# Performance work log

Hardware: AMD Instinct MI355X
Metric: run time of the kernel (lower is better)

The kernel has to match this reference:

```python
import jax, jax.numpy as jnp
import numpy as np

B, C, CI, HM, HC = 4, 64, 32, 128, 64  # batch, in_channels, inter_channels, main HW, cross HW
BN_EPS = 1e-5


def conv1x1(x, w, b):
    # x: [B,Cin,H,W], w: [Cout,Cin], b: [Cout]
    return jnp.einsum('bchw,oc->bohw', x, w) + b[None, :, None, None]


def _lin_coords(n_in, n_out):
    # PyTorch bilinear, align_corners=False: src = (i+0.5)*scale - 0.5, clamped
    scale = n_in / n_out
    src = (jnp.arange(n_out, dtype=jnp.float32) + 0.5) * scale - 0.5
    src = jnp.clip(src, 0.0, n_in - 1)
    i0 = jnp.floor(src).astype(jnp.int32)
    i1 = jnp.minimum(i0 + 1, n_in - 1)
    w = src - i0.astype(jnp.float32)
    return i0, i1, w


def resize_bilinear(x, h_out, w_out):
    # x: [B,C,H,W] -> [B,C,h_out,w_out], matches torch F.interpolate(mode='bilinear', align_corners=False)
    _, _, h_in, w_in = x.shape
    i0, i1, wh = _lin_coords(h_in, h_out)
    x = x[:, :, i0, :] * (1.0 - wh)[None, None, :, None] + x[:, :, i1, :] * wh[None, None, :, None]
    j0, j1, ww = _lin_coords(w_in, w_out)
    x = x[:, :, :, j0] * (1.0 - ww)[None, None, None, :] + x[:, :, :, j1] * ww[None, None, None, :]
    return x


def setup_inputs() -> dict:
    key = jax.random.key(0)
    ks = jax.random.split(key, 12)
    p = lambda k, shape, s=0.05: jax.random.normal(k, shape, dtype=jnp.float32) * s
    return {
        'main_feature': jax.random.normal(ks[0], (B, C, HM, HM), dtype=jnp.float32),
        'cross_feature': jax.random.normal(ks[1], (B, C, HC, HC), dtype=jnp.float32),
        'g_w': p(ks[2], (CI, C)), 'g_b': p(ks[3], (CI,)),
        'theta_w': p(ks[4], (CI, C)), 'theta_b': p(ks[5], (CI,)),
        'phi_w': p(ks[6], (CI, C)), 'phi_b': p(ks[7], (CI,)),
        'w_w': p(ks[8], (C, CI)), 'w_b': p(ks[9], (C,)),
        'bn_gamma': 1.0 + p(ks[10], (C,)), 'bn_beta': p(ks[11], (C,)),
    }


def reference(main_feature, cross_feature, g_w, g_b, theta_w, theta_b,
              phi_w, phi_b, w_w, w_b, bn_gamma, bn_beta):
    b, _, hc, wc = cross_feature.shape
    hm = main_feature.shape[2]
    # g(cross) -> [B, Nc, Ci]
    x = conv1x1(cross_feature, g_w, g_b).reshape(b, CI, -1).transpose(0, 2, 1)
    # theta(cross) -> [B, Ci, Nc]
    y = conv1x1(cross_feature, theta_w, theta_b).reshape(b, CI, -1)
    # phi(resize(main -> cross size)) -> [B, Nc, Ci]
    z = resize_bilinear(main_feature, hc, hc)
    z = conv1x1(z, phi_w, phi_b).reshape(b, CI, -1).transpose(0, 2, 1)
    # unscaled attention: [B, Nc, Nc]
    f = jnp.einsum('bnc,bcm->bnm', x, y)
    attn = jax.nn.softmax(f, axis=-1)
    out = jnp.einsum('bnm,bmc->bnc', attn, z)           # [B, Nc, Ci]
    out = out.transpose(0, 2, 1).reshape(b, CI, hc, wc)  # [B, Ci, Hc, Wc]
    # W: 1x1 conv + BatchNorm2d (training mode: batch statistics, biased var)
    out = conv1x1(out, w_w, w_b)
    mean = out.mean(axis=(0, 2, 3), keepdims=True)
    var = out.var(axis=(0, 2, 3), keepdims=True)
    out = (out - mean) * jax.lax.rsqrt(var + BN_EPS)
    out = out * bn_gamma[None, :, None, None] + bn_beta[None, :, None, None]
    out = resize_bilinear(out, hm, hm)
    return out + main_feature
```

## Files before the change

kernel.cpp:

```cpp
#include <hip/hip_runtime.h>
#include <hip/hip_bf16.h>


typedef __attribute__((ext_vector_type(8))) short bf16x8;
typedef __attribute__((ext_vector_type(4))) float f32x4;
typedef __attribute__((ext_vector_type(16))) float f32x16;

#define LOG2E 1.4426950408889634f

static __device__ __forceinline__ unsigned short f2bf_bits(float x) {
    __hip_bfloat16 h = __float2bfloat16(x);
    return *(unsigned short*)&h;
}
static __device__ __forceinline__ unsigned int pk2bf(float a, float b) {
    __hip_bfloat162 h = __float22bfloat162_rn(make_float2(a, b));
    return *(unsigned int*)&h;
}

static __device__ __forceinline__ void softmax_pack(
    const f32x16& s, float& den, bf16x8& ap1, bf16x8& ap2)
{
    float e[16];
#pragma unroll
    for (int r = 0; r < 16; ++r) e[r] = __builtin_amdgcn_exp2f(s[r]);
    den += (((e[0]+e[1])+(e[2]+e[3])) + ((e[4]+e[5])+(e[6]+e[7])))
         + (((e[8]+e[9])+(e[10]+e[11])) + ((e[12]+e[13])+(e[14]+e[15])));
    uint4 t1 = make_uint4(pk2bf(e[0],e[1]), pk2bf(e[2],e[3]),
                          pk2bf(e[4],e[5]), pk2bf(e[6],e[7]));
    uint4 t2 = make_uint4(pk2bf(e[8],e[9]), pk2bf(e[10],e[11]),
                          pk2bf(e[12],e[13]), pk2bf(e[14],e[15]));
    ap1 = *(bf16x8*)&t1; ap2 = *(bf16x8*)&t2;
}

__global__ __launch_bounds__(256) void qkv_kernel(
    const float* __restrict__ cross, const float* __restrict__ mainf,
    const float* __restrict__ g_w,  const float* __restrict__ g_b,
    const float* __restrict__ th_w, const float* __restrict__ th_b,
    const float* __restrict__ ph_w, const float* __restrict__ ph_b,
    __hip_bfloat16* __restrict__ Qb, __hip_bfloat16* __restrict__ Kf,
    __hip_bfloat16* __restrict__ Vf)
{
    __shared__ __align__(16) float xs[64][128];
    const int kind = blockIdx.x >> 7;
    const int sub  = blockIdx.x & 127;
    const int b    = sub >> 5;
    const int n0   = (sub & 31) << 7;
    const int tid  = threadIdx.x;
    const float* w  = (kind == 0) ? g_w : (kind == 1) ? th_w : ph_w;
    const float* bs = (kind == 0) ? g_b : (kind == 1) ? th_b : ph_b;

    if (kind < 2) {
        const float* src = cross + (((size_t)(b * 64)) << 12) + n0;
        const int jr = (tid & 31) << 2, c0 = tid >> 5;
#pragma unroll
        for (int it = 0; it < 8; ++it) {
            int c = (it << 3) | c0;
            *(float4*)&xs[c][jr] = *(const float4*)(src + ((size_t)c << 12) + jr);
        }
    } else {
        const int px = tid & 127, chh = tid >> 7;
        const int n = n0 + px;
        const int i2 = (n >> 6) << 1, j2 = (n & 63) << 1;
        const float* src = mainf + (((size_t)(b * 64)) << 14) + i2 * 128 + j2;
#pragma unroll 4
        for (int cc = 0; cc < 32; ++cc) {
            int c = (chh << 5) | cc;
            const float2 a = *(const float2*)(src + ((size_t)c << 14));
            const float2 d = *(const float2*)(src + ((size_t)c << 14) + 128);
            xs[c][px] = 0.25f * ((a.x + a.y) + (d.x + d.y));
        }
    }
    __syncthreads();

    if (kind < 2) {
        const int px = tid & 127, cih = tid >> 7, ci0 = cih << 4;
        float acc[16];
#pragma unroll
        for (int j = 0; j < 16; ++j) acc[j] = bs[ci0 + j];
#pragma unroll 4
        for (int c = 0; c < 64; ++c) {
            float x = xs[c][px];
#pragma unroll
            for (int j = 0; j < 16; ++j)
                acc[j] = fmaf(w[((ci0 + j) << 6) + c], x, acc[j]);
        }
        const int n = n0 + px;
        const int chunk = n >> 5, kk = n & 31;
        if (kind == 0) {
#pragma unroll
            for (int j = 0; j < 16; ++j) acc[j] *= LOG2E;
            unsigned int u[8];
#pragma unroll
            for (int i = 0; i < 8; ++i)
                u[i] = (unsigned int)f2bf_bits(acc[2 * i]) |
                       ((unsigned int)f2bf_bits(acc[2 * i + 1]) << 16);
            uint4* d4 = (uint4*)(Qb + (size_t)((b << 12) + n) * 32 + ci0);
            d4[0] = make_uint4(u[0], u[1], u[2], u[3]);
            d4[1] = make_uint4(u[4], u[5], u[6], u[7]);
        } else {
            unsigned int u[8];
#pragma unroll
            for (int i = 0; i < 8; ++i)
                u[i] = (unsigned int)f2bf_bits(acc[2 * i]) |
                       ((unsigned int)f2bf_bits(acc[2 * i + 1]) << 16);
            const int q = (kk & ~12) | ((kk & 4) << 1) | ((kk & 8) >> 1);
            char* base = (char*)Kf + ((((size_t)(b << 7) | chunk) << 11) | (cih << 10));
            *(uint4*)(base + (q << 4))          = make_uint4(u[0], u[1], u[2], u[3]);
            *(uint4*)(base + ((32 + q) << 4))   = make_uint4(u[4], u[5], u[6], u[7]);
        }
    } else {
        const int cip = tid & 15, o = tid >> 4;
        const int c0 = cip << 1;
        const int pxb = o << 3;
        float a0[8], a1[8];
        const float b0 = bs[c0], b1 = bs[c0 + 1];
#pragma unroll
        for (int i = 0; i < 8; ++i) { a0[i] = b0; a1[i] = b1; }
#pragma unroll 4
        for (int c = 0; c < 64; ++c) {
            const float w0 = w[(c0 << 6) + c], w1 = w[((c0 + 1) << 6) + c];
            const float4 xa = *(const float4*)&xs[c][pxb];
            const float4 xb = *(const float4*)&xs[c][pxb + 4];
            a0[0] = fmaf(w0, xa.x, a0[0]); a0[1] = fmaf(w0, xa.y, a0[1]);
            a0[2] = fmaf(w0, xa.z, a0[2]); a0[3] = fmaf(w0, xa.w, a0[3]);
            a0[4] = fmaf(w0, xb.x, a0[4]); a0[5] = fmaf(w0, xb.y, a0[5]);
            a0[6] = fmaf(w0, xb.z, a0[6]); a0[7] = fmaf(w0, xb.w, a0[7]);
            a1[0] = fmaf(w1, xa.x, a1[0]); a1[1] = fmaf(w1, xa.y, a1[1]);
            a1[2] = fmaf(w1, xa.z, a1[2]); a1[3] = fmaf(w1, xa.w, a1[3]);
            a1[4] = fmaf(w1, xb.x, a1[4]); a1[5] = fmaf(w1, xb.y, a1[5]);
            a1[6] = fmaf(w1, xb.z, a1[6]); a1[7] = fmaf(w1, xb.w, a1[7]);
        }
        unsigned int u0[4], u1[4];
#pragma unroll
        for (int i = 0; i < 4; ++i) {
            u0[i] = (unsigned int)f2bf_bits(a0[2 * i]) |
                    ((unsigned int)f2bf_bits(a0[2 * i + 1]) << 16);
            u1[i] = (unsigned int)f2bf_bits(a1[2 * i]) |
                    ((unsigned int)f2bf_bits(a1[2 * i + 1]) << 16);
        }
        const int n = n0 + pxb;
        const int chunk = n >> 5;
        const int j = (o >> 1) & 1, hh = o & 1;
        char* base = (char*)Vf + (((size_t)((b << 7) | chunk)) << 11)
                   + (j << 10) + (hh << 9) + (c0 << 4);
        *(uint4*)base        = make_uint4(u0[0], u0[1], u0[2], u0[3]);
        *(uint4*)(base + 16) = make_uint4(u1[0], u1[1], u1[2], u1[3]);
    }
}

__global__ __launch_bounds__(256) void attn_part(
    const __hip_bfloat16* __restrict__ Qb, const __hip_bfloat16* __restrict__ Kf,
    const __hip_bfloat16* __restrict__ Vf,
    float* __restrict__ pnum, float* __restrict__ pden)
{
    __shared__ __align__(16) float redbuf[4][3][64][16];
    __shared__ float denarr[4][3][64];
    const int tid = threadIdx.x, lane = tid & 63, w = tid >> 6;
    const int q = lane & 31, h = lane >> 5;
    const int b = blockIdx.y, qbase = blockIdx.x << 7, eighth = blockIdx.z;

    const __hip_bfloat16* QrowA = Qb + (((size_t)(b << 12) + qbase + q) << 5);
    const bf16x8 bq1A = *(const bf16x8*)(QrowA + 8 * h);
    const bf16x8 bq2A = *(const bf16x8*)(QrowA + 16 + 8 * h);
    const bf16x8 bq1B = *(const bf16x8*)(QrowA + (32 << 5) + 8 * h);
    const bf16x8 bq2B = *(const bf16x8*)(QrowA + (32 << 5) + 16 + 8 * h);
    const bf16x8 bq1C = *(const bf16x8*)(QrowA + (64 << 5) + 8 * h);
    const bf16x8 bq2C = *(const bf16x8*)(QrowA + (64 << 5) + 16 + 8 * h);
    const bf16x8 bq1D = *(const bf16x8*)(QrowA + (96 << 5) + 8 * h);
    const bf16x8 bq2D = *(const bf16x8*)(QrowA + (96 << 5) + 16 + 8 * h);

    const char* Kc = (const char*)Kf +
        ((size_t)((b << 7) | (eighth << 4) | (w << 2)) << 11) + (lane << 4);
    const char* Vc = (const char*)Vf +
        ((size_t)((b << 7) | (eighth << 4) | (w << 2)) << 11) + (lane << 4);
#define LDK1(c) (*(const bf16x8*)(Kc + ((c) << 11)))
#define LDK2(c) (*(const bf16x8*)(Kc + ((c) << 11) + 1024))
#define LDV1(c) (*(const bf16x8*)(Vc + ((c) << 11)))
#define LDV2(c) (*(const bf16x8*)(Vc + ((c) << 11) + 1024))

    f32x16 accA, accB, accC, accD;
#pragma unroll
    for (int r = 0; r < 16; ++r) { accA[r]=0.f; accB[r]=0.f; accC[r]=0.f; accD[r]=0.f; }
    const f32x16 z16 = accA;
    float denA = 0.f, denB = 0.f, denC = 0.f, denD = 0.f;

    bf16x8 a1c = LDK1(0), a2c = LDK2(0);
    bf16x8 vb1 = LDV1(0), vb2 = LDV2(0);
    bf16x8 a1n = LDK1(1), a2n = LDK2(1);
    bf16x8 vn1 = LDV1(1), vn2 = LDV2(1);
    bf16x8 apA1, apA2, apB1, apB2, apC1, apC2, apD1, apD2, vp1, vp2;

    {
        f32x16 s = __builtin_amdgcn_mfma_f32_32x32x16_bf16(a1c, bq1A, z16, 0, 0, 0);
        s = __builtin_amdgcn_mfma_f32_32x32x16_bf16(a2c, bq2A, s, 0, 0, 0);
        softmax_pack(s, denA, apA1, apA2);
        s = __builtin_amdgcn_mfma_f32_32x32x16_bf16(a1c, bq1B, z16, 0, 0, 0);
        s = __builtin_amdgcn_mfma_f32_32x32x16_bf16(a2c, bq2B, s, 0, 0, 0);
        softmax_pack(s, denB, apB1, apB2);
        s = __builtin_amdgcn_mfma_f32_32x32x16_bf16(a1c, bq1C, z16, 0, 0, 0);
        s = __builtin_amdgcn_mfma_f32_32x32x16_bf16(a2c, bq2C, s, 0, 0, 0);
        softmax_pack(s, denC, apC1, apC2);
        s = __builtin_amdgcn_mfma_f32_32x32x16_bf16(a1c, bq1D, z16, 0, 0, 0);
        s = __builtin_amdgcn_mfma_f32_32x32x16_bf16(a2c, bq2D, s, 0, 0, 0);
        softmax_pack(s, denD, apD1, apD2);
    }

#pragma unroll
    for (int ch = 1; ch < 4; ++ch) {
        const int kn = (ch + 1) & 3;
        vp1 = vb1; vp2 = vb2;
        vb1 = vn1; vb2 = vn2;
        a1c = a1n; a2c = a2n;
        a1n = LDK1(kn); a2n = LDK2(kn);
        vn1 = LDV1(kn); vn2 = LDV2(kn);

        accA = __builtin_amdgcn_mfma_f32_32x32x16_bf16(apA1, vp1, accA, 0, 0, 0);
        accA = __builtin_amdgcn_mfma_f32_32x32x16_bf16(apA2, vp2, accA, 0, 0, 0);
        accB = __builtin_amdgcn_mfma_f32_32x32x16_bf16(apB1, vp1, accB, 0, 0, 0);
        accB = __builtin_amdgcn_mfma_f32_32x32x16_bf16(apB2, vp2, accB, 0, 0, 0);
        accC = __builtin_amdgcn_mfma_f32_32x32x16_bf16(apC1, vp1, accC, 0, 0, 0);
        accC = __builtin_amdgcn_mfma_f32_32x32x16_bf16(apC2, vp2, accC, 0, 0, 0);
        accD = __builtin_amdgcn_mfma_f32_32x32x16_bf16(apD1, vp1, accD, 0, 0, 0);
        accD = __builtin_amdgcn_mfma_f32_32x32x16_bf16(apD2, vp2, accD, 0, 0, 0);

        f32x16 s = __builtin_amdgcn_mfma_f32_32x32x16_bf16(a1c, bq1A, z16, 0, 0, 0);
        s = __builtin_amdgcn_mfma_f32_32x32x16_bf16(a2c, bq2A, s, 0, 0, 0);
        softmax_pack(s, denA, apA1, apA2);
        s = __builtin_amdgcn_mfma_f32_32x32x16_bf16(a1c, bq1B, z16, 0, 0, 0);
        s = __builtin_amdgcn_mfma_f32_32x32x16_bf16(a2c, bq2B, s, 0, 0, 0);
        softmax_pack(s, denB, apB1, apB2);
        s = __builtin_amdgcn_mfma_f32_32x32x16_bf16(a1c, bq1C, z16, 0, 0, 0);
        s = __builtin_amdgcn_mfma_f32_32x32x16_bf16(a2c, bq2C, s, 0, 0, 0);
        softmax_pack(s, denC, apC1, apC2);
        s = __builtin_amdgcn_mfma_f32_32x32x16_bf16(a1c, bq1D, z16, 0, 0, 0);
        s = __builtin_amdgcn_mfma_f32_32x32x16_bf16(a2c, bq2D, s, 0, 0, 0);
        softmax_pack(s, denD, apD1, apD2);
    }
    accA = __builtin_amdgcn_mfma_f32_32x32x16_bf16(apA1, vb1, accA, 0, 0, 0);
    accA = __builtin_amdgcn_mfma_f32_32x32x16_bf16(apA2, vb2, accA, 0, 0, 0);
    accB = __builtin_amdgcn_mfma_f32_32x32x16_bf16(apB1, vb1, accB, 0, 0, 0);
    accB = __builtin_amdgcn_mfma_f32_32x32x16_bf16(apB2, vb2, accB, 0, 0, 0);
    accC = __builtin_amdgcn_mfma_f32_32x32x16_bf16(apC1, vb1, accC, 0, 0, 0);
    accC = __builtin_amdgcn_mfma_f32_32x32x16_bf16(apC2, vb2, accC, 0, 0, 0);
    accD = __builtin_amdgcn_mfma_f32_32x32x16_bf16(apD1, vb1, accD, 0, 0, 0);
    accD = __builtin_amdgcn_mfma_f32_32x32x16_bf16(apD2, vb2, accD, 0, 0, 0);
#undef LDK1
#undef LDK2
#undef LDV1
#undef LDV2

    denA += __shfl_xor(denA, 32);
    denB += __shfl_xor(denB, 32);
    denC += __shfl_xor(denC, 32);
    denD += __shfl_xor(denD, 32);

    if (w) {
        float d[4] = {denA, denB, denC, denD};
        const f32x16* av[4] = {&accA, &accB, &accC, &accD};
#pragma unroll
        for (int T = 0; T < 4; ++T) {
            float* rb = &redbuf[T][w - 1][lane][0];
            f32x4* rb4 = (f32x4*)rb;
            const f32x16& a = *av[T];
#pragma unroll
            for (int p = 0; p < 4; ++p) {
                f32x4 t = {a[4*p], a[4*p+1], a[4*p+2], a[4*p+3]};
                rb4[p] = t;
            }
            denarr[T][w - 1][lane] = d[T];
        }
    }
    __syncthreads();
    if (w == 0) {
        const int tbase = (((eighth << 2) | b) << 7) | (blockIdx.x << 2);
        float d[4] = {denA, denB, denC, denD};
        f32x16* av[4] = {&accA, &accB, &accC, &accD};
#pragma unroll
        for (int T = 0; T < 4; ++T) {
            f32x16& a = *av[T];
#pragma unroll
            for (int ww = 0; ww < 3; ++ww) {
                const float* rb = &redbuf[T][ww][lane][0];
                const f32x4* rb4 = (const f32x4*)rb;
#pragma unroll
                for (int p = 0; p < 4; ++p) {
                    f32x4 t = rb4[p];
                    a[4*p] += t[0]; a[4*p+1] += t[1];
                    a[4*p+2] += t[2]; a[4*p+3] += t[3];
                }
                d[T] += denarr[T][ww][lane];
            }
            float* pn = pnum + ((size_t)(tbase + T) << 10);
#pragma unroll
            for (int r = 0; r < 16; ++r) {
                int qr = (r & 3) + 8 * (r >> 2) + 4 * h;
                pn[(qr << 5) + q] = a[r];
            }
            if (h == 0) pden[((tbase + T) << 5) + q] = d[T];
        }
    }
}

__global__ __launch_bounds__(256) void attn_combine(
    const float* __restrict__ pnum, const float* __restrict__ pden,
    const float* __restrict__ w_w, const float* __restrict__ w_b,
    float* __restrict__ out2, float2* __restrict__ pstats)
{
    __shared__ __align__(16) float obuf[32][36];
    const int tid = threadIdx.x;
    const int b = blockIdx.y, qbase = blockIdx.x << 5;

#pragma unroll
    for (int k = 0; k < 4; ++k) {
        int e = tid + (k << 8);
        int qr = e >> 5;
        float num = 0.f, den = 0.f;
#pragma unroll
        for (int eighth = 0; eighth < 8; ++eighth) {
            int tile = (((eighth << 2) | b) << 7) | blockIdx.x;
            num += pnum[((size_t)tile << 10) + e];
            den += pden[(tile << 5) + qr];
        }
        obuf[qr][e & 31] = num * (1.0f / den);
    }
    __syncthreads();

    const int qq = tid & 31, cog = tid >> 5;
    float ov[32];
    const float4* orow = (const float4*)&obuf[qq][0];
#pragma unroll
    for (int k4 = 0; k4 < 8; ++k4) {
        float4 t = orow[k4];
        ov[4*k4] = t.x; ov[4*k4+1] = t.y; ov[4*k4+2] = t.z; ov[4*k4+3] = t.w;
    }
    float* dstbase = out2 + (((size_t)(b << 6)) << 12) + qbase + qq;
    const int tileidx = (b << 7) | blockIdx.x;
#pragma unroll
    for (int kk = 0; kk < 8; ++kk) {
        int co = (kk << 3) | cog;
        const float4* wr = (const float4*)&w_w[co << 5];
        float acc2 = w_b[co];
#pragma unroll
        for (int k4 = 0; k4 < 8; ++k4) {
            float4 t = wr[k4];
            acc2 = fmaf(t.x, ov[4*k4],   acc2);
            acc2 = fmaf(t.y, ov[4*k4+1], acc2);
            acc2 = fmaf(t.z, ov[4*k4+2], acc2);
            acc2 = fmaf(t.w, ov[4*k4+3], acc2);
        }
        dstbase[(size_t)co << 12] = acc2;
        float s1 = acc2, s2 = acc2 * acc2;
#pragma unroll
        for (int m = 1; m < 32; m <<= 1) {
            s1 += __shfl_xor(s1, m);
            s2 += __shfl_xor(s2, m);
        }
        if (qq == 0) pstats[(co << 9) | tileidx] = make_float2(s1, s2);
    }
}

__global__ __launch_bounds__(256) void up_kernel(
    const float* __restrict__ out2, const float2* __restrict__ pstats,
    const float* __restrict__ gamma, const float* __restrict__ beta,
    const float* __restrict__ mainf, float* __restrict__ out)
{
    int gid = blockIdx.x * 256 + threadIdx.x;
    int j4 = (gid & 31) << 2;
    int i  = (gid >> 5) & 127;
    int co = (gid >> 12) & 63;
    int b  = gid >> 18;
    int t  = threadIdx.x;

    __shared__ float rs[256], rs2[256];
    {
        float2 p0 = pstats[(co << 9) | t];
        float2 p1 = pstats[(co << 9) | (t + 256)];
        rs[t] = p0.x + p1.x; rs2[t] = p0.y + p1.y;
    }
    __syncthreads();
    for (int off = 128; off > 0; off >>= 1) {
        if (t < off) { rs[t] += rs[t + off]; rs2[t] += rs2[t + off]; }
        __syncthreads();
    }
    float sm = rs[0], sq = rs2[0];

    float mean = sm * (1.0f / 16384.0f);
    float var  = sq * (1.0f / 16384.0f) - mean * mean;
    float inv  = rsqrtf(var + 1e-5f);
    float scale = gamma[co] * inv;
    float shift = beta[co] - mean * scale;

    int ih = i >> 1;
    int k0, k1; float wi;
    if (i & 1)       { k0 = ih;     k1 = (ih < 63) ? ih + 1 : 63; wi = 0.25f; }
    else if (ih == 0){ k0 = 0;      k1 = 0;                       wi = 0.0f;  }
    else             { k0 = ih - 1; k1 = ih;                      wi = 0.75f; }

    const float* p0r = out2 + ((size_t)((b << 6) | co) << 12) + (k0 << 6);
    const float* p1r = out2 + ((size_t)((b << 6) | co) << 12) + (k1 << 6);

    float res[4];
#pragma unroll
    for (int jj = 0; jj < 4; ++jj) {
        int j = j4 | jj;
        int il = j >> 1;
        int l0, l1; float wj;
        if (j & 1)       { l0 = il;     l1 = (il < 63) ? il + 1 : 63; wj = 0.25f; }
        else if (il == 0){ l0 = 0;      l1 = 0;                       wj = 0.0f;  }
        else             { l0 = il - 1; l1 = il;                      wj = 0.75f; }
        float v00 = p0r[l0], v01 = p0r[l1];
        float v10 = p1r[l0], v11 = p1r[l1];
        float top = v00 + wj * (v01 - v00);
        float bot = v10 + wj * (v11 - v10);
        float v = top + wi * (bot - top);
        res[jj] = fmaf(v, scale, shift);
    }
    size_t idx = (((size_t)((b << 6) | co)) << 14) + (i << 7) + j4;
    float4 m4 = *(const float4*)(mainf + idx);
    *(float4*)(out + idx) = make_float4(res[0] + m4.x, res[1] + m4.y,
                                        res[2] + m4.z, res[3] + m4.w);
}

extern "C" void kernel_launch(void* const* d_in, const int* in_sizes, int n_in,
                              void* d_out, int out_size, void* d_ws, size_t ws_size,
                              hipStream_t stream)
{
    const float* mainf = (const float*)d_in[0];
    const float* cross = (const float*)d_in[1];
    const float* g_w   = (const float*)d_in[2];
    const float* g_b   = (const float*)d_in[3];
    const float* th_w  = (const float*)d_in[4];
    const float* th_b  = (const float*)d_in[5];
    const float* ph_w  = (const float*)d_in[6];
    const float* ph_b  = (const float*)d_in[7];
    const float* w_w   = (const float*)d_in[8];
    const float* w_b   = (const float*)d_in[9];
    const float* gamma = (const float*)d_in[10];
    const float* beta  = (const float*)d_in[11];
    float* out = (float*)d_out;

    __hip_bfloat16* Qb = (__hip_bfloat16*)d_ws;
    __hip_bfloat16* Kf = Qb + 524288;
    __hip_bfloat16* Vf = Kf + 524288;
    float* out2   = (float*)(Vf + 524288);
    float* pnum   = out2 + 1048576;
    float* pden   = pnum + 4194304;
    float2* pstats = (float2*)(pden + 131072);

    qkv_kernel<<<384, 256, 0, stream>>>(cross, mainf, g_w, g_b, th_w, th_b,
                                        ph_w, ph_b, Qb, Kf, Vf);
    attn_part<<<dim3(32, 4, 8), 256, 0, stream>>>(Qb, Kf, Vf, pnum, pden);
    attn_combine<<<dim3(128, 4), 256, 0, stream>>>(pnum, pden, w_w, w_b,
                                                   out2, pstats);
    up_kernel<<<4096, 256, 0, stream>>>(out2, pstats, gamma, beta, mainf, out);
}
```

Measured before the change: 140.8 us.

## Fuse attention combine into attn_part via last-block atomic counter

Removes the separate attn_combine launch. Each attn_part block bumps a per-(batch, query-block) counter, and the last of the eight key-split blocks reduces the partial numerators and denominators, applies the W projection and writes the BN partial stats. The counters are zeroed in qkv_kernel. This saves one kernel launch and its tail, but the combine work now runs serialised in only 128 last-arriving blocks, each handling four query tiles, which can lengthen the tail of attn_part.

```diff
diff --git a/kernel.cpp b/kernel.cpp
--- a/kernel.cpp
+++ b/kernel.cpp
@@ -38,7 +38,7 @@
     const float* __restrict__ th_w, const float* __restrict__ th_b,
     const float* __restrict__ ph_w, const float* __restrict__ ph_b,
     __hip_bfloat16* __restrict__ Qb, __hip_bfloat16* __restrict__ Kf,
-    __hip_bfloat16* __restrict__ Vf)
+    __hip_bfloat16* __restrict__ Vf, unsigned int* __restrict__ cnt)
 {
     __shared__ __align__(16) float xs[64][128];
     const int kind = blockIdx.x >> 7;
@@ -48,6 +48,8 @@
     const int tid  = threadIdx.x;
     const float* w  = (kind == 0) ? g_w : (kind == 1) ? th_w : ph_w;
     const float* bs = (kind == 0) ? g_b : (kind == 1) ? th_b : ph_b;
+
+    if (blockIdx.x == 0 && tid < 128) cnt[tid] = 0;
 
     if (kind < 2) {
         const float* src = cross + (((size_t)(b * 64)) << 12) + n0;
@@ -151,10 +153,14 @@
 __global__ __launch_bounds__(256) void attn_part(
     const __hip_bfloat16* __restrict__ Qb, const __hip_bfloat16* __restrict__ Kf,
     const __hip_bfloat16* __restrict__ Vf,
-    float* __restrict__ pnum, float* __restrict__ pden)
+    float* __restrict__ pnum, float* __restrict__ pden,
+    const float* __restrict__ w_w, const float* __restrict__ w_b,
+    float* __restrict__ out2, float2* __restrict__ pstats,
+    unsigned int* __restrict__ cnt)
 {
     __shared__ __align__(16) float redbuf[4][3][64][16];
     __shared__ float denarr[4][3][64];
+    __shared__ unsigned int lastFlag;
     const int tid = threadIdx.x, lane = tid & 63, w = tid >> 6;
     const int q = lane & 31, h = lane >> 5;
     const int b = blockIdx.y, qbase = blockIdx.x << 7, eighth = blockIdx.z;
@@ -299,63 +305,70 @@
             if (h == 0) pden[((tbase + T) << 5) + q] = d[T];
         }
     }
-}
-
-__global__ __launch_bounds__(256) void attn_combine(
-    const float* __restrict__ pnum, const float* __restrict__ pden,
-    const float* __restrict__ w_w, const float* __restrict__ w_b,
-    float* __restrict__ out2, float2* __restrict__ pstats)
-{
-    __shared__ __align__(16) float obuf[32][36];
-    const int tid = threadIdx.x;
-    const int b = blockIdx.y, qbase = blockIdx.x << 5;
-
-#pragma unroll
-    for (int k = 0; k < 4; ++k) {
-        int e = tid + (k << 8);
-        int qr = e >> 5;
-        float num = 0.f, den = 0.f;
-#pragma unroll
-        for (int eighth = 0; eighth < 8; ++eighth) {
-            int tile = (((eighth << 2) | b) << 7) | blockIdx.x;
-            num += pnum[((size_t)tile << 10) + e];
-            den += pden[(tile << 5) + qr];
-        }
-        obuf[qr][e & 31] = num * (1.0f / den);
+
+    __threadfence();
+    __syncthreads();
+    if (tid == 0)
+        lastFlag = (atomicAdd(&cnt[(b << 5) | blockIdx.x], 1u) == 7u);
+    __syncthreads();
+    if (!lastFlag) return;
+    __threadfence();
+
+    float (*obuf)[32][36] = (float (*)[32][36])redbuf;
+#pragma unroll
+    for (int T = 0; T < 4; ++T) {
+        const int qtile = (blockIdx.x << 2) | T;
+#pragma unroll
+        for (int k = 0; k < 4; ++k) {
+            int e = tid + (k << 8);
+            int qr = e >> 5;
+            float num = 0.f, den = 0.f;
+#pragma unroll
+            for (int E = 0; E < 8; ++E) {
+                int tile = (((E << 2) | b) << 7) | qtile;
+                num += pnum[((size_t)tile << 10) + e];
+                den += pden[(tile << 5) + qr];
+            }
+            obuf[T][qr][e & 31] = num * (1.0f / den);
+        }
     }
     __syncthreads();
 
     const int qq = tid & 31, cog = tid >> 5;
-    float ov[32];
-    const float4* orow = (const float4*)&obuf[qq][0];
-#pragma unroll
-    for (int k4 = 0; k4 < 8; ++k4) {
-        float4 t = orow[k4];
-        ov[4*k4] = t.x; ov[4*k4+1] = t.y; ov[4*k4+2] = t.z; ov[4*k4+3] = t.w;
-    }
-    float* dstbase = out2 + (((size_t)(b << 6)) << 12) + qbase + qq;
-    const int tileidx = (b << 7) | blockIdx.x;
-#pragma unroll
-    for (int kk = 0; kk < 8; ++kk) {
-        int co = (kk << 3) | cog;
-        const float4* wr = (const float4*)&w_w[co << 5];
-        float acc2 = w_b[co];
+#pragma unroll
+    for (int T = 0; T < 4; ++T) {
+        const int qtile = (blockIdx.x << 2) | T;
+        float ov[32];
+        const float4* orow = (const float4*)&obuf[T][qq][0];
 #pragma unroll
         for (int k4 = 0; k4 < 8; ++k4) {
-            float4 t = wr[k4];
-            acc2 = fmaf(t.x, ov[4*k4],   acc2);
-            acc2 = fmaf(t.y, ov[4*k4+1], acc2);
-            acc2 = fmaf(t.z, ov[4*k4+2], acc2);
-            acc2 = fmaf(t.w, ov[4*k4+3], acc2);
-        }
-        dstbase[(size_t)co << 12] = acc2;
-        float s1 = acc2, s2 = acc2 * acc2;
-#pragma unroll
-        for (int m = 1; m < 32; m <<= 1) {
-            s1 += __shfl_xor(s1, m);
-            s2 += __shfl_xor(s2, m);
-        }
-        if (qq == 0) pstats[(co << 9) | tileidx] = make_float2(s1, s2);
+            float4 t = orow[k4];
+            ov[4*k4] = t.x; ov[4*k4+1] = t.y; ov[4*k4+2] = t.z; ov[4*k4+3] = t.w;
+        }
+        float* dstbase = out2 + (((size_t)(b << 6)) << 12) + (qtile << 5) + qq;
+        const int tileidx = (b << 7) | qtile;
+#pragma unroll
+        for (int kk = 0; kk < 8; ++kk) {
+            int co = (kk << 3) | cog;
+            const float4* wr = (const float4*)&w_w[co << 5];
+            float acc2 = w_b[co];
+#pragma unroll
+            for (int k4 = 0; k4 < 8; ++k4) {
+                float4 t = wr[k4];
+                acc2 = fmaf(t.x, ov[4*k4],   acc2);
+                acc2 = fmaf(t.y, ov[4*k4+1], acc2);
+                acc2 = fmaf(t.z, ov[4*k4+2], acc2);
+                acc2 = fmaf(t.w, ov[4*k4+3], acc2);
+            }
+            dstbase[(size_t)co << 12] = acc2;
+            float s1 = acc2, s2 = acc2 * acc2;
+#pragma unroll
+            for (int m = 1; m < 32; m <<= 1) {
+                s1 += __shfl_xor(s1, m);
+                s2 += __shfl_xor(s2, m);
+            }
+            if (qq == 0) pstats[(co << 9) | tileidx] = make_float2(s1, s2);
+        }
     }
 }
 
@@ -446,11 +459,11 @@
     float* pnum   = out2 + 1048576;
     float* pden   = pnum + 4194304;
     float2* pstats = (float2*)(pden + 131072);
+    unsigned int* cnt = (unsigned int*)(pstats + 32768);
 
     qkv_kernel<<<384, 256, 0, stream>>>(cross, mainf, g_w, g_b, th_w, th_b,
-                                        ph_w, ph_b, Qb, Kf, Vf);
-    attn_part<<<dim3(32, 4, 8), 256, 0, stream>>>(Qb, Kf, Vf, pnum, pden);
-    attn_combine<<<dim3(128, 4), 256, 0, stream>>>(pnum, pden, w_w, w_b,
-                                                   out2, pstats);
+                                        ph_w, ph_b, Qb, Kf, Vf, cnt);
+    attn_part<<<dim3(32, 4, 8), 256, 0, stream>>>(Qb, Kf, Vf, pnum, pden,
+                                                  w_w, w_b, out2, pstats, cnt);
     up_kernel<<<4096, 256, 0, stream>>>(out2, pstats, gamma, beta, mainf, out);
 }
```

After: 249.5 us. 77.2% more time.
